# Performance work log

Measured on AMD Instinct MI355X. Metric: run time of the kernel, lower is better.

Reference implementation:

```python
import jax, jax.numpy as jnp
import numpy as np

N = 100000      # nodes
E = 1000000     # edges (before self-loops)
IN_DIM = 256
H = 4           # heads
C = 32          # out_dim per head
NEG_SLOPE = 0.2  # PyG GATConv default negative_slope


def setup_inputs() -> dict:
    key = jax.random.key(0)
    ks = jax.random.split(key, 6)
    x = jax.random.normal(ks[0], (N, IN_DIM), jnp.float32)
    W = jax.random.normal(ks[1], (IN_DIM, H * C), jnp.float32) * (1.0 / np.sqrt(IN_DIM))
    a_src = jax.random.normal(ks[2], (H, C), jnp.float32) * 0.1
    a_dst = jax.random.normal(ks[3], (H, C), jnp.float32) * 0.1
    bias = jnp.zeros((H * C,), jnp.float32)
    edge_index = jax.random.randint(ks[4], (2, E), 0, N, dtype=jnp.int32)
    return {"x": x, "W": W, "a_src": a_src, "a_dst": a_dst, "bias": bias,
            "edge_index": edge_index}


def reference(x, W, a_src, a_dst, bias, edge_index):
    n = x.shape[0]
    # PyG GATConv default: add self-loops
    loops = jnp.arange(n, dtype=edge_index.dtype)
    src = jnp.concatenate([edge_index[0], loops])  # [E+N]
    dst = jnp.concatenate([edge_index[1], loops])  # [E+N]
    # linear transform -> [N, H, C]
    h = (x @ W).reshape(n, H, C)
    # per-node attention logits
    alpha_s = jnp.einsum('nhc,hc->nh', h, a_src)  # [N, H]
    alpha_d = jnp.einsum('nhc,hc->nh', h, a_dst)  # [N, H]
    # per-edge score, LeakyReLU
    e = jax.nn.leaky_relu(alpha_s[src] + alpha_d[dst], NEG_SLOPE)  # [E+N, H]
    # segment softmax over incoming edges of each destination node
    m = jax.lax.stop_gradient(jax.ops.segment_max(e, dst, num_segments=n))
    p = jnp.exp(e - m[dst])
    s = jax.ops.segment_sum(p, dst, num_segments=n)
    alpha = p / (s[dst] + 1e-16)  # [E+N, H]
    # weighted scatter-add of source features
    out = jax.ops.segment_sum(alpha[:, :, None] * h[src], dst, num_segments=n)  # [N, H, C]
    out = out.reshape(n, H * C) + bias
    return jnp.tanh(out)
```

## Files before the change

### kernel.cpp

```cpp
#include <hip/hip_runtime.h>

#define IN_DIM 256
#define HC     128
#define NHEAD  4
#define NEG    0.2f
#define AS     264
#define BKT    1024
#define NBMAX  128
#define EPT    16
#define BE     4096

typedef __attribute__((ext_vector_type(8))) short short8v;
typedef __attribute__((ext_vector_type(4))) float f32x4;
typedef __attribute__((ext_vector_type(4))) unsigned short ushort4v;

__device__ __forceinline__ unsigned short bf16_rn(float f) {
    unsigned u = __builtin_bit_cast(unsigned, f);
    return (unsigned short)((u + 0x7fffu + ((u >> 16) & 1u)) >> 16);
}
__device__ __forceinline__ float bf16_to_f32(unsigned short b) {
    unsigned u = ((unsigned)b) << 16;
    return __builtin_bit_cast(float, u);
}
__device__ __forceinline__ float bf16_lo(unsigned v) {
    return __builtin_bit_cast(float, v << 16);
}
__device__ __forceinline__ float bf16_hi(unsigned v) {
    return __builtin_bit_cast(float, v & 0xffff0000u);
}
__device__ __forceinline__ float fast_tanh(float x) {
    float t = __expf(2.f * x);
    return fmaf(-2.f, __builtin_amdgcn_rcpf(t + 1.f), 1.f);
}
__device__ __forceinline__ float lrelu(float e) {
    return fmaxf(e, NEG * e);
}

__global__ void pack_w_kernel(const float* __restrict__ W,
                              unsigned short* __restrict__ w_hi) {
    int t = blockIdx.x * 256 + threadIdx.x;
    if (t >= 8 * 8 * 64) return;
    int l  = t & 63;
    int ct = (t >> 6) & 7;
    int s  = t >> 9;
    int kbase = s * 32 + (l >> 4) * 8;
    int col   = ct * 16 + (l & 15);
    size_t base = (size_t)t * 8;
#pragma unroll
    for (int e = 0; e < 8; ++e)
        w_hi[base + e] = bf16_rn(W[(size_t)(kbase + e) * HC + col]);
}

__global__ __launch_bounds__(512) void gemm_mfma_kernel(const float* __restrict__ x,
                                                        const unsigned short* __restrict__ w_hi,
                                                        const float* __restrict__ a_src,
                                                        const float* __restrict__ a_dst,
                                                        unsigned short* __restrict__ h_bf,
                                                        float* __restrict__ alpha_s,
                                                        float* __restrict__ alpha_d, int n) {
    __shared__ unsigned short s_hi[64][AS];
    __shared__ unsigned short s_lo[64][AS];
    __shared__ float pS[64][4];
    __shared__ float pD[64][4];

    const int tid = threadIdx.x;
    const int l   = tid & 63;
    const int wv  = tid >> 6;
    const int row0 = blockIdx.x * 64;

    const float4* x4 = reinterpret_cast<const float4*>(x);
#pragma unroll
    for (int i = 0; i < 8; ++i) {
        int f = tid + i * 512;
        int row = f >> 6, c4 = f & 63;
        float4 v = make_float4(0.f, 0.f, 0.f, 0.f);
        if (row0 + row < n) v = x4[(size_t)(row0 + row) * 64 + c4];
        float e[4] = {v.x, v.y, v.z, v.w};
        ushort4v hi, lo;
#pragma unroll
        for (int q = 0; q < 4; ++q) {
            unsigned short h16 = bf16_rn(e[q]);
            hi[q] = h16;
            lo[q] = bf16_rn(e[q] - bf16_to_f32(h16));
        }
        *reinterpret_cast<ushort4v*>(&s_hi[row][c4 * 4]) = hi;
        *reinterpret_cast<ushort4v*>(&s_lo[row][c4 * 4]) = lo;
    }
    __syncthreads();

    const int ct_g = wv & 3;
    const int rt_g = wv >> 2;
    const int rrow = l & 15;
    const int koff = (l >> 4) * 8;

    f32x4 acc[2][2];
#pragma unroll
    for (int a = 0; a < 2; ++a)
#pragma unroll
        for (int b = 0; b < 2; ++b) acc[a][b] = (f32x4){0.f, 0.f, 0.f, 0.f};

    for (int s = 0; s < 8; ++s) {
        short8v bh[2];
#pragma unroll
        for (int c = 0; c < 2; ++c) {
            int ct = ct_g * 2 + c;
            bh[c] = *reinterpret_cast<const short8v*>(w_hi + ((size_t)(s * 8 + ct) * 64 + l) * 8);
        }
#pragma unroll
        for (int r = 0; r < 2; ++r) {
            int arow = rt_g * 32 + r * 16 + rrow;
            short8v ah = *reinterpret_cast<const short8v*>(&s_hi[arow][koff + s * 32]);
            short8v al = *reinterpret_cast<const short8v*>(&s_lo[arow][koff + s * 32]);
#pragma unroll
            for (int c = 0; c < 2; ++c) {
                acc[r][c] = __builtin_amdgcn_mfma_f32_16x16x32_bf16(ah, bh[c], acc[r][c], 0, 0, 0);
                acc[r][c] = __builtin_amdgcn_mfma_f32_16x16x32_bf16(al, bh[c], acc[r][c], 0, 0, 0);
            }
        }
    }

#pragma unroll
    for (int r = 0; r < 2; ++r) {
#pragma unroll
        for (int c = 0; c < 2; ++c) {
            int col = (ct_g * 2 + c) * 16 + (l & 15);
#pragma unroll
            for (int q = 0; q < 4; ++q) {
                int row = row0 + rt_g * 32 + r * 16 + (l >> 4) * 4 + q;
                if (row < n) h_bf[(size_t)row * HC + col] = bf16_rn(acc[r][c][q]);
            }
        }
    }

    float asc[2], adc[2];
#pragma unroll
    for (int c = 0; c < 2; ++c) {
        int col = (ct_g * 2 + c) * 16 + (l & 15);
        asc[c] = a_src[col];
        adc[c] = a_dst[col];
    }
#pragma unroll
    for (int r = 0; r < 2; ++r) {
#pragma unroll
        for (int q = 0; q < 4; ++q) {
            float vS = acc[r][0][q] * asc[0] + acc[r][1][q] * asc[1];
            float vD = acc[r][0][q] * adc[0] + acc[r][1][q] * adc[1];
#pragma unroll
            for (int m = 1; m < 16; m <<= 1) {
                vS += __shfl_xor(vS, m);
                vD += __shfl_xor(vD, m);
            }
            if ((l & 15) == 0) {
                int rl = rt_g * 32 + r * 16 + (l >> 4) * 4 + q;
                pS[rl][ct_g] = vS;
                pD[rl][ct_g] = vD;
            }
        }
    }
    __syncthreads();
    if (tid < 256) {
        int rl = tid >> 2, h = tid & 3;
        int row = row0 + rl;
        if (row < n) {
            alpha_s[(size_t)row * 4 + h] = pS[rl][h];
            alpha_d[(size_t)row * 4 + h] = pD[rl][h];
        }
    }
}

__global__ __launch_bounds__(256) void bucket_hist_kernel(const int* __restrict__ ei,
                                                          int* __restrict__ bucket_cnt,
                                                          int E, int nb) {
    __shared__ int lh[NBMAX];
    int tid = threadIdx.x;
    if (tid < NBMAX) lh[tid] = 0;
    __syncthreads();
    int base = blockIdx.x * BE;
#pragma unroll
    for (int i = 0; i < EPT; ++i) {
        int e = base + i * 256 + tid;
        if (e < E) atomicAdd(&lh[ei[E + e] >> 10], 1);
    }
    __syncthreads();
    if (tid < nb && lh[tid]) atomicAdd(&bucket_cnt[tid], lh[tid]);
}

__global__ __launch_bounds__(128) void bucket_scan_kernel(const int* __restrict__ bucket_cnt,
                                                          int* __restrict__ bucket_base,
                                                          int* __restrict__ bucket_cursor,
                                                          int nb) {
    __shared__ int ws0[1];
    int t = threadIdx.x;
    int v = (t < nb) ? bucket_cnt[t] : 0;
    int lane = t & 63, wd = t >> 6;
    int x = v;
#pragma unroll
    for (int off = 1; off < 64; off <<= 1) {
        int y = __shfl_up(x, off);
        if (lane >= off) x += y;
    }
    if (wd == 0 && lane == 63) ws0[0] = x;
    __syncthreads();
    int wo = wd ? ws0[0] : 0;
    int excl = wo + x - v;
    if (t < nb) { bucket_base[t] = excl; bucket_cursor[t] = excl; }
    if (t == 127) bucket_base[nb] = wo + x;
}

__global__ __launch_bounds__(256) void bucket_scatter_kernel(const int* __restrict__ ei,
                                                             int* __restrict__ bucket_cursor,
                                                             unsigned* __restrict__ bucket_data,
                                                             int E, int nb) {
    __shared__ int lh[NBMAX];
    __shared__ int lofs[NBMAX];
    __shared__ int gofs[NBMAX];
    __shared__ int ws0[1];
    __shared__ unsigned buf[BE];

    int tid = threadIdx.x;
    if (tid < NBMAX) lh[tid] = 0;
    __syncthreads();

    int base = blockIdx.x * BE;
    int bb[EPT]; unsigned wv[EPT]; int rr[EPT];
#pragma unroll
    for (int i = 0; i < EPT; ++i) {
        int e = base + i * 256 + tid;
        if (e < E) {
            int src = ei[e];
            int dst = ei[E + e];
            bb[i] = dst >> 10;
            wv[i] = (unsigned)src | ((unsigned)(dst & 1023) << 17);
            rr[i] = atomicAdd(&lh[bb[i]], 1);
        } else bb[i] = -1;
    }
    __syncthreads();

    int v_ = 0, x_ = 0;
    int lane = tid & 63, wd = tid >> 6;
    if (tid < NBMAX) {
        v_ = lh[tid]; x_ = v_;
#pragma unroll
        for (int off = 1; off < 64; off <<= 1) {
            int y = __shfl_up(x_, off);
            if (lane >= off) x_ += y;
        }
        if (wd == 0 && lane == 63) ws0[0] = x_;
    }
    __syncthreads();
    if (tid < NBMAX) {
        int wo = wd ? ws0[0] : 0;
        lofs[tid] = wo + x_ - v_;
    }
    __syncthreads();

#pragma unroll
    for (int i = 0; i < EPT; ++i)
        if (bb[i] >= 0) buf[lofs[bb[i]] + rr[i]] = wv[i];
    if (tid < nb) gofs[tid] = lh[tid] ? atomicAdd(&bucket_cursor[tid], lh[tid]) : 0;
    __syncthreads();

    int wid = tid >> 6;
    for (int bk = wid; bk < nb; bk += 4) {
        int lo = lofs[bk], cnt = lh[bk], g = gofs[bk];
        for (int j = lane; j < cnt; j += 64)
            bucket_data[g + j] = buf[lo + j];
    }
}

__global__ __launch_bounds__(1024) void bucket_build_kernel(const int* __restrict__ bucket_base,
                                                            const unsigned* __restrict__ bucket_data,
                                                            int* __restrict__ deg,
                                                            int* __restrict__ row_start,
                                                            int* __restrict__ csr_src, int n) {
    __shared__ int lc[BKT];
    __shared__ int sc[BKT];
    __shared__ int wsum[16];

    int b = blockIdx.x;
    int base = bucket_base[b];
    int end  = bucket_base[b + 1];
    int t = threadIdx.x;

    lc[t] = 0;
    __syncthreads();
    for (int i = base + t; i < end; i += 1024)
        atomicAdd(&lc[bucket_data[i] >> 17], 1);
    __syncthreads();

    int val = lc[t];
    int lane = t & 63, wd = t >> 6;
    int x = val;
#pragma unroll
    for (int off = 1; off < 64; off <<= 1) {
        int y = __shfl_up(x, off);
        if (lane >= off) x += y;
    }
    if (lane == 63) wsum[wd] = x;
    __syncthreads();
    if (wd == 0 && lane < 16) {
        int y = wsum[lane];
#pragma unroll
        for (int off = 1; off < 16; off <<= 1) {
            int z = __shfl_up(y, off);
            if (lane >= off) y += z;
        }
        wsum[lane] = y;
    }
    __syncthreads();
    int wo = wd ? wsum[wd - 1] : 0;
    int excl = wo + x - val;
    sc[t] = excl;
    int v = b * BKT + t;
    if (v < n) { deg[v] = val; row_start[v] = base + excl; }
    lc[t] = 0;
    __syncthreads();

    for (int i = base + t; i < end; i += 1024) {
        unsigned w = bucket_data[i];
        int d = w >> 17;
        int src = (int)(w & 0x1FFFFu);
        int p = atomicAdd(&lc[d], 1);
        csr_src[base + sc[d] + p] = src;
    }
}

__global__ __launch_bounds__(256) void gather_kernel(const int* __restrict__ row_start,
                                                     const int* __restrict__ deg,
                                                     const int* __restrict__ csr_src,
                                                     const float* __restrict__ alpha_s,
                                                     const float* __restrict__ alpha_d,
                                                     const unsigned short* __restrict__ h_bf,
                                                     const float* __restrict__ bias,
                                                     float* __restrict__ out, int n) {
    int lane = threadIdx.x & 63;
    int wid  = threadIdx.x >> 6;
    int v = blockIdx.x * 4 + wid;
    if (v >= n) return;
    int start = row_start[v];
    int cnt = deg[v];
    int head = lane >> 4;

    const unsigned* hb = reinterpret_cast<const unsigned*>(h_bf);

    float adH = alpha_d[(size_t)v * 4 + head];
    float asH = alpha_s[(size_t)v * 4 + head];
    float pself = __expf(lrelu(asH + adH));
    unsigned hv0 = hb[((unsigned)v << 6) + lane];
    float s = pself;
    float accx = pself * bf16_lo(hv0);
    float accy = pself * bf16_hi(hv0);

    int j = 0;
    for (; j + 8 <= cnt; j += 8) {
        int s0 = csr_src[start + j + 0];
        int s1 = csr_src[start + j + 1];
        int s2 = csr_src[start + j + 2];
        int s3 = csr_src[start + j + 3];
        int s4 = csr_src[start + j + 4];
        int s5 = csr_src[start + j + 5];
        int s6 = csr_src[start + j + 6];
        int s7 = csr_src[start + j + 7];
        float a0 = alpha_s[(size_t)s0 * 4 + head];
        float a1 = alpha_s[(size_t)s1 * 4 + head];
        float a2 = alpha_s[(size_t)s2 * 4 + head];
        float a3 = alpha_s[(size_t)s3 * 4 + head];
        float a4 = alpha_s[(size_t)s4 * 4 + head];
        float a5 = alpha_s[(size_t)s5 * 4 + head];
        float a6 = alpha_s[(size_t)s6 * 4 + head];
        float a7 = alpha_s[(size_t)s7 * 4 + head];
        unsigned h0 = hb[((unsigned)s0 << 6) + lane];
        unsigned h1 = hb[((unsigned)s1 << 6) + lane];
        unsigned h2 = hb[((unsigned)s2 << 6) + lane];
        unsigned h3 = hb[((unsigned)s3 << 6) + lane];
        unsigned h4 = hb[((unsigned)s4 << 6) + lane];
        unsigned h5 = hb[((unsigned)s5 << 6) + lane];
        unsigned h6 = hb[((unsigned)s6 << 6) + lane];
        unsigned h7 = hb[((unsigned)s7 << 6) + lane];
        float w0 = __expf(lrelu(a0 + adH));
        float w1 = __expf(lrelu(a1 + adH));
        float w2 = __expf(lrelu(a2 + adH));
        float w3 = __expf(lrelu(a3 + adH));
        float w4 = __expf(lrelu(a4 + adH));
        float w5 = __expf(lrelu(a5 + adH));
        float w6 = __expf(lrelu(a6 + adH));
        float w7 = __expf(lrelu(a7 + adH));
        s += w0 + w1 + w2 + w3 + w4 + w5 + w6 + w7;
        accx = fmaf(w0, bf16_lo(h0), accx); accy = fmaf(w0, bf16_hi(h0), accy);
        accx = fmaf(w1, bf16_lo(h1), accx); accy = fmaf(w1, bf16_hi(h1), accy);
        accx = fmaf(w2, bf16_lo(h2), accx); accy = fmaf(w2, bf16_hi(h2), accy);
        accx = fmaf(w3, bf16_lo(h3), accx); accy = fmaf(w3, bf16_hi(h3), accy);
        accx = fmaf(w4, bf16_lo(h4), accx); accy = fmaf(w4, bf16_hi(h4), accy);
        accx = fmaf(w5, bf16_lo(h5), accx); accy = fmaf(w5, bf16_hi(h5), accy);
        accx = fmaf(w6, bf16_lo(h6), accx); accy = fmaf(w6, bf16_hi(h6), accy);
        accx = fmaf(w7, bf16_lo(h7), accx); accy = fmaf(w7, bf16_hi(h7), accy);
    }
    for (; j + 4 <= cnt; j += 4) {
        int s0 = csr_src[start + j + 0];
        int s1 = csr_src[start + j + 1];
        int s2 = csr_src[start + j + 2];
        int s3 = csr_src[start + j + 3];
        float a0 = alpha_s[(size_t)s0 * 4 + head];
        float a1 = alpha_s[(size_t)s1 * 4 + head];
        float a2 = alpha_s[(size_t)s2 * 4 + head];
        float a3 = alpha_s[(size_t)s3 * 4 + head];
        unsigned h0 = hb[((unsigned)s0 << 6) + lane];
        unsigned h1 = hb[((unsigned)s1 << 6) + lane];
        unsigned h2 = hb[((unsigned)s2 << 6) + lane];
        unsigned h3 = hb[((unsigned)s3 << 6) + lane];
        float w0 = __expf(lrelu(a0 + adH));
        float w1 = __expf(lrelu(a1 + adH));
        float w2 = __expf(lrelu(a2 + adH));
        float w3 = __expf(lrelu(a3 + adH));
        s += w0 + w1 + w2 + w3;
        accx = fmaf(w0, bf16_lo(h0), accx); accy = fmaf(w0, bf16_hi(h0), accy);
        accx = fmaf(w1, bf16_lo(h1), accx); accy = fmaf(w1, bf16_hi(h1), accy);
        accx = fmaf(w2, bf16_lo(h2), accx); accy = fmaf(w2, bf16_hi(h2), accy);
        accx = fmaf(w3, bf16_lo(h3), accx); accy = fmaf(w3, bf16_hi(h3), accy);
    }
    for (; j < cnt; ++j) {
        int s0 = csr_src[start + j];
        float a0 = alpha_s[(size_t)s0 * 4 + head];
        unsigned h0 = hb[((unsigned)s0 << 6) + lane];
        float w0 = __expf(lrelu(a0 + adH));
        s += w0;
        accx = fmaf(w0, bf16_lo(h0), accx);
        accy = fmaf(w0, bf16_hi(h0), accy);
    }

    float invH = __builtin_amdgcn_rcpf(s + 1e-16f);
    float2 b = reinterpret_cast<const float2*>(bias)[lane];
    float2 o;
    o.x = fast_tanh(fmaf(accx, invH, b.x));
    o.y = fast_tanh(fmaf(accy, invH, b.y));
    reinterpret_cast<float2*>(out)[(size_t)v * 64 + lane] = o;
}

extern "C" void kernel_launch(void* const* d_in, const int* in_sizes, int n_in,
                              void* d_out, int out_size, void* d_ws, size_t ws_size,
                              hipStream_t stream) {
    const float* x     = (const float*)d_in[0];
    const float* W     = (const float*)d_in[1];
    const float* a_src = (const float*)d_in[2];
    const float* a_dst = (const float*)d_in[3];
    const float* bias  = (const float*)d_in[4];
    const int*   ei    = (const int*)d_in[5];

    const int n = in_sizes[0] / IN_DIM;
    const int E = in_sizes[5] / 2;
    const int nb = (n + BKT - 1) / BKT;

    float* ws = (float*)d_ws;
    size_t off = 0;
    unsigned short* h_bf = (unsigned short*)(ws + off); off += (size_t)n * HC / 2;
    float* alpha_s = ws + off; off += (size_t)n * NHEAD;
    float* alpha_d = ws + off; off += (size_t)n * NHEAD;
    unsigned short* w_hi = (unsigned short*)(ws + off); off += 16384;
    int* ibase        = (int*)(ws + off);
    int* deg          = ibase;
    int* row_start    = ibase + n;
    int* bucket_cnt   = ibase + 2 * (size_t)n;
    int* bucket_base  = bucket_cnt + NBMAX;
    int* bucket_cursor= bucket_base + NBMAX + 1;
    unsigned* bucket_data = (unsigned*)(bucket_cursor + NBMAX);
    int* csr_src      = (int*)(bucket_data + E);

    float* out = (float*)d_out;

    const int nblkE = (E + BE - 1) / BE;

    hipMemsetAsync(bucket_cnt, 0, NBMAX * sizeof(int), stream);

    pack_w_kernel<<<16, 256, 0, stream>>>(W, w_hi);
    gemm_mfma_kernel<<<(n + 63) / 64, 512, 0, stream>>>(x, w_hi, a_src, a_dst,
                                                        h_bf, alpha_s, alpha_d, n);

    bucket_hist_kernel<<<nblkE, 256, 0, stream>>>(ei, bucket_cnt, E, nb);
    bucket_scan_kernel<<<1, 128, 0, stream>>>(bucket_cnt, bucket_base, bucket_cursor, nb);
    bucket_scatter_kernel<<<nblkE, 256, 0, stream>>>(ei, bucket_cursor, bucket_data, E, nb);
    bucket_build_kernel<<<nb, 1024, 0, stream>>>(bucket_base, bucket_data,
                                                 deg, row_start, csr_src, n);

    gather_kernel<<<(n + 3) / 4, 256, 0, stream>>>(row_start, deg, csr_src,
                                                   alpha_s, alpha_d, h_bf, bias, out, n);
}
```

Baseline: 153.3 us.

## Drop bf16 hi/lo split of x in GEMM and use XOR-swizzled LDS layout

The GEMM previously split each x value into high and low bf16 parts and ran two MFMAs per tile to recover near-fp32 accuracy. Now x is rounded once to bf16, which halves the MFMA work, the LDS footprint and the LDS reads. The padded row layout is replaced by an XOR-swizzled layout to avoid LDS bank conflicts. In exchange, h and the attention logits lose precision, which could push results past tolerance.

```diff
diff --git a/kernel.cpp b/kernel.cpp
--- a/kernel.cpp
+++ b/kernel.cpp
@@ -4,7 +4,6 @@
 #define HC     128
 #define NHEAD  4
 #define NEG    0.2f
-#define AS     264
 #define BKT    1024
 #define NBMAX  128
 #define EPT    16
@@ -58,8 +57,7 @@
                                                         unsigned short* __restrict__ h_bf,
                                                         float* __restrict__ alpha_s,
                                                         float* __restrict__ alpha_d, int n) {
-    __shared__ unsigned short s_hi[64][AS];
-    __shared__ unsigned short s_lo[64][AS];
+    __shared__ unsigned short s_bf[64 * 256];
     __shared__ float pS[64][4];
     __shared__ float pD[64][4];
 
@@ -71,27 +69,23 @@
     const float4* x4 = reinterpret_cast<const float4*>(x);
 #pragma unroll
     for (int i = 0; i < 8; ++i) {
-        int f = tid + i * 512;
-        int row = f >> 6, c4 = f & 63;
+        int row = i * 8 + wv;
+        int c4  = l;
         float4 v = make_float4(0.f, 0.f, 0.f, 0.f);
         if (row0 + row < n) v = x4[(size_t)(row0 + row) * 64 + c4];
-        float e[4] = {v.x, v.y, v.z, v.w};
-        ushort4v hi, lo;
-#pragma unroll
-        for (int q = 0; q < 4; ++q) {
-            unsigned short h16 = bf16_rn(e[q]);
-            hi[q] = h16;
-            lo[q] = bf16_rn(e[q] - bf16_to_f32(h16));
-        }
-        *reinterpret_cast<ushort4v*>(&s_hi[row][c4 * 4]) = hi;
-        *reinterpret_cast<ushort4v*>(&s_lo[row][c4 * 4]) = lo;
+        ushort4v b;
+        b[0] = bf16_rn(v.x); b[1] = bf16_rn(v.y);
+        b[2] = bf16_rn(v.z); b[3] = bf16_rn(v.w);
+        int slot = (c4 >> 1) ^ (row & 7);
+        int uidx = row * 256 + (slot << 3) + ((c4 & 1) << 2);
+        *reinterpret_cast<ushort4v*>(&s_bf[uidx]) = b;
     }
     __syncthreads();
 
     const int ct_g = wv & 3;
     const int rt_g = wv >> 2;
     const int rrow = l & 15;
-    const int koff = (l >> 4) * 8;
+    const int kq   = l >> 4;
 
     f32x4 acc[2][2];
 #pragma unroll
@@ -109,13 +103,12 @@
 #pragma unroll
         for (int r = 0; r < 2; ++r) {
             int arow = rt_g * 32 + r * 16 + rrow;
-            short8v ah = *reinterpret_cast<const short8v*>(&s_hi[arow][koff + s * 32]);
-            short8v al = *reinterpret_cast<const short8v*>(&s_lo[arow][koff + s * 32]);
-#pragma unroll
-            for (int c = 0; c < 2; ++c) {
+            int c16  = kq + s * 4;
+            int uidx = arow * 256 + ((c16 ^ (arow & 7)) << 3);
+            short8v ah = *reinterpret_cast<const short8v*>(&s_bf[uidx]);
+#pragma unroll
+            for (int c = 0; c < 2; ++c)
                 acc[r][c] = __builtin_amdgcn_mfma_f32_16x16x32_bf16(ah, bh[c], acc[r][c], 0, 0, 0);
-                acc[r][c] = __builtin_amdgcn_mfma_f32_16x16x32_bf16(al, bh[c], acc[r][c], 0, 0, 0);
-            }
         }
     }
 
```

Result: faster. 146.5 us (-4.5%).
